# Kernel optimization log

Measured on AMD Instinct MI355X. Metric: run time of the kernel, lower is better.

## Reference

```python
import jax, jax.numpy as jnp
import numpy as np

EMBED_DIM = 768
HIDDEN_DIM = 768
ASPECT_NUM = 32
BATCH = 256


def setup_inputs() -> dict:
    key = jax.random.key(0)
    k1, k2, k3, k4, k5, k6, k7 = jax.random.split(key, 7)
    s = 0.02
    return {
        "v_X": jax.random.normal(k1, (BATCH, EMBED_DIM), dtype=jnp.float32),
        "v_H": jax.random.normal(k2, (BATCH, HIDDEN_DIM), dtype=jnp.float32),
        "aspect_ids": jax.random.randint(k3, (BATCH,), 0, ASPECT_NUM, dtype=jnp.int64),
        "W1_embs": s * jax.random.normal(k4, (ASPECT_NUM, (EMBED_DIM + HIDDEN_DIM) * HIDDEN_DIM), dtype=jnp.float32),
        "b1_embs": s * jax.random.normal(k5, (ASPECT_NUM, HIDDEN_DIM), dtype=jnp.float32),
        "W2_embs": s * jax.random.normal(k6, (ASPECT_NUM, HIDDEN_DIM * 2), dtype=jnp.float32),
        "b2_embs": s * jax.random.normal(k7, (ASPECT_NUM, 2), dtype=jnp.float32),
    }


def reference(v_X, v_H, aspect_ids, W1_embs, b1_embs, W2_embs, b2_embs):
    batch = v_X.shape[0]
    V = jnp.concatenate([v_X, v_H], axis=-1)  # (B, E+H)
    W1 = W1_embs[aspect_ids].reshape(batch, EMBED_DIM + HIDDEN_DIM, HIDDEN_DIM)
    b1 = b1_embs[aspect_ids]                  # (B, H)
    W2 = W2_embs[aspect_ids].reshape(batch, HIDDEN_DIM, 2)
    b2 = b2_embs[aspect_ids]                  # (B, 2)
    out1 = jax.nn.relu(jnp.einsum('bd,bdh->bh', V, W1) + b1)  # per-sample GEMV
    logits = jnp.einsum('bh,bht->bt', out1, W2) + b2
    return logits
```

## Files before the change

kernel.cpp:

```cpp
#include <hip/hip_runtime.h>
#include <hip/hip_bf16.h>

#define EMBED 768
#define HID 768
#define DTOT 1536
#define NASP 32
#define BATCHN 256
#define CH 16
#define MAXCHUNK 48
#define NTILE 6
#define DSPLIT 8
#define DROWS (DTOT / DSPLIT)

__global__ __launch_bounds__(256, 4) void gemv1_kernel(
    const float* __restrict__ vX, const float* __restrict__ vH,
    const float* __restrict__ W1, const int* __restrict__ aspect_ids,
    float* __restrict__ part)
{
    __shared__ int wcnt[4][NASP];
    __shared__ int basearr[NASP];
    __shared__ int countsarr[NASP];
    __shared__ int chasp[MAXCHUNK];
    __shared__ int smpall[MAXCHUNK][CH];
    __shared__ int nchunks_s;
    __shared__ __align__(16) float Vs[DROWS][CH];
    __shared__ __align__(16) float4 red[512];

    int t = threadIdx.x;
    int lane = t & 63;
    int wave = t >> 6;
    int myaid = aspect_ids[t];

    unsigned long long mymask = 0ull;
    for (int a = 0; a < NASP; ++a) {
        bool p = (myaid == a);
        unsigned long long m = __ballot(p);
        if (p) mymask = m;
        if (lane == a) wcnt[wave][a] = __popcll(m);
    }
    __syncthreads();
    if (t < NASP) {
        int ctot = wcnt[0][t] + wcnt[1][t] + wcnt[2][t] + wcnt[3][t];
        countsarr[t] = ctot;
        int nc = (ctot + CH - 1) / CH;
        int incl = nc;
        #pragma unroll
        for (int off = 1; off < NASP; off <<= 1) {
            int v = __shfl_up(incl, off, 64);
            if (t >= off) incl += v;
        }
        int base = incl - nc;
        basearr[t] = base;
        for (int j = 0; j < nc; ++j) chasp[base + j] = t;
        if (t == NASP - 1) nchunks_s = incl;
    }
    __syncthreads();
    {
        int pre = 0;
        for (int w2 = 0; w2 < wave; ++w2) pre += wcnt[w2][myaid];
        int r = pre + __popcll(mymask & ((1ull << lane) - 1ull));
        int c = basearr[myaid] + r / CH;
        smpall[c][r % CH] = t;
    }
    __syncthreads();

    int bid = blockIdx.x;
    int chunk = bid / (NTILE * DSPLIT);
    if (chunk >= nchunks_s) return;
    int rem  = bid % (NTILE * DSPLIT);
    int tile = rem / DSPLIT;
    int dsp  = rem % DSPLIT;

    int aspect = chasp[chunk];
    int cnt = countsarr[aspect] - CH * (chunk - basearr[aspect]);
    if (cnt > CH) cnt = CH;

    int dbase = dsp * DROWS;

    #pragma unroll
    for (int r = 0; r < 3; ++r) {
        int id = t + r * 256;
        int s = id & (CH - 1);
        int f = id >> 4;
        int smp = (s < cnt) ? smpall[chunk][s] : smpall[chunk][0];
        int d = dbase + f * 4;
        const float* src = (dbase < EMBED)
            ? (vX + (size_t)smp * EMBED + d)
            : (vH + (size_t)smp * HID + (d - EMBED));
        float4 v = *(const float4*)src;
        Vs[f * 4 + 0][s] = v.x;
        Vs[f * 4 + 1][s] = v.y;
        Vs[f * 4 + 2][s] = v.z;
        Vs[f * 4 + 3][s] = v.w;
    }
    __syncthreads();

    int c32 = t & 31;
    int dg  = t >> 5;
    int h   = tile * 128 + c32 * 4;

    const float* wp = W1 + (size_t)aspect * ((size_t)DTOT * HID)
                         + (size_t)(dbase + dg) * HID + h;

    float4 acc[CH];
    #pragma unroll
    for (int s = 0; s < CH; ++s) { acc[s].x = acc[s].y = acc[s].z = acc[s].w = 0.f; }

    #pragma unroll 4
    for (int k = 0; k < DROWS / 8; ++k) {
        float4 w = *(const float4*)wp;
        wp += 8 * HID;
        int d = k * 8 + dg;
        float4 va = *(const float4*)&Vs[d][0];
        float4 vb = *(const float4*)&Vs[d][4];
        float4 vc = *(const float4*)&Vs[d][8];
        float4 vd = *(const float4*)&Vs[d][12];
        acc[0].x  += va.x * w.x; acc[0].y  += va.x * w.y; acc[0].z  += va.x * w.z; acc[0].w  += va.x * w.w;
        acc[1].x  += va.y * w.x; acc[1].y  += va.y * w.y; acc[1].z  += va.y * w.z; acc[1].w  += va.y * w.w;
        acc[2].x  += va.z * w.x; acc[2].y  += va.z * w.y; acc[2].z  += va.z * w.z; acc[2].w  += va.z * w.w;
        acc[3].x  += va.w * w.x; acc[3].y  += va.w * w.y; acc[3].z  += va.w * w.z; acc[3].w  += va.w * w.w;
        acc[4].x  += vb.x * w.x; acc[4].y  += vb.x * w.y; acc[4].z  += vb.x * w.z; acc[4].w  += vb.x * w.w;
        acc[5].x  += vb.y * w.x; acc[5].y  += vb.y * w.y; acc[5].z  += vb.y * w.z; acc[5].w  += vb.y * w.w;
        acc[6].x  += vb.z * w.x; acc[6].y  += vb.z * w.y; acc[6].z  += vb.z * w.z; acc[6].w  += vb.z * w.w;
        acc[7].x  += vb.w * w.x; acc[7].y  += vb.w * w.y; acc[7].z  += vb.w * w.z; acc[7].w  += vb.w * w.w;
        acc[8].x  += vc.x * w.x; acc[8].y  += vc.x * w.y; acc[8].z  += vc.x * w.z; acc[8].w  += vc.x * w.w;
        acc[9].x  += vc.y * w.x; acc[9].y  += vc.y * w.y; acc[9].z  += vc.y * w.z; acc[9].w  += vc.y * w.w;
        acc[10].x += vc.z * w.x; acc[10].y += vc.z * w.y; acc[10].z += vc.z * w.z; acc[10].w += vc.z * w.w;
        acc[11].x += vc.w * w.x; acc[11].y += vc.w * w.y; acc[11].z += vc.w * w.z; acc[11].w += vc.w * w.w;
        acc[12].x += vd.x * w.x; acc[12].y += vd.x * w.y; acc[12].z += vd.x * w.z; acc[12].w += vd.x * w.w;
        acc[13].x += vd.y * w.x; acc[13].y += vd.y * w.y; acc[13].z += vd.y * w.z; acc[13].w += vd.y * w.w;
        acc[14].x += vd.z * w.x; acc[14].y += vd.z * w.y; acc[14].z += vd.z * w.z; acc[14].w += vd.z * w.w;
        acc[15].x += vd.w * w.x; acc[15].y += vd.w * w.y; acc[15].z += vd.w * w.z; acc[15].w += vd.w * w.w;
    }

    size_t dsp_off = (size_t)dsp * BATCHN * HID;
    #pragma unroll
    for (int sp = 0; sp < CH / 2; ++sp) {
        __syncthreads();
        red[t]       = acc[2 * sp + 0];
        red[256 + t] = acc[2 * sp + 1];
        __syncthreads();
        if (t < 64) {
            int half = t >> 5;
            int l32  = t & 31;
            int s = 2 * sp + half;
            float4 sum = red[half * 256 + l32];
            #pragma unroll
            for (int g = 1; g < 8; ++g) {
                float4 o = red[half * 256 + g * 32 + l32];
                sum.x += o.x; sum.y += o.y; sum.z += o.z; sum.w += o.w;
            }
            if (s < cnt) {
                int smp = smpall[chunk][s];
                *(float4*)&part[dsp_off + (size_t)smp * HID + tile * 128 + l32 * 4] = sum;
            }
        }
    }
}

__global__ __launch_bounds__(64) void head_kernel(
    const float* __restrict__ part, const int* __restrict__ aspect_ids,
    const float* __restrict__ b1, const float* __restrict__ W2,
    const float* __restrict__ b2, float* __restrict__ logits)
{
    int s = blockIdx.x;
    int t = threadIdx.x;
    int a = aspect_ids[s];
    const float* w2 = W2 + (size_t)a * HID * 2;
    const float* b1p = b1 + (size_t)a * HID;
    float p0 = 0.f, p1 = 0.f;
    #pragma unroll
    for (int j = 0; j < HID / 64; ++j) {
        int hh = t + j * 64;
        float o = 0.f;
        #pragma unroll
        for (int p = 0; p < DSPLIT; ++p) {
            o += part[(size_t)p * BATCHN * HID + (size_t)s * HID + hh];
        }
        o = fmaxf(o + b1p[hh], 0.f);
        p0 += o * w2[hh * 2 + 0];
        p1 += o * w2[hh * 2 + 1];
    }
    #pragma unroll
    for (int off = 32; off > 0; off >>= 1) {
        p0 += __shfl_down(p0, off, 64);
        p1 += __shfl_down(p1, off, 64);
    }
    if (t == 0) {
        logits[s * 2 + 0] = p0 + b2[a * 2 + 0];
        logits[s * 2 + 1] = p1 + b2[a * 2 + 1];
    }
}

extern "C" void kernel_launch(void* const* d_in, const int* in_sizes, int n_in,
                              void* d_out, int out_size, void* d_ws, size_t ws_size,
                              hipStream_t stream) {
    const float* vX  = (const float*)d_in[0];
    const float* vH  = (const float*)d_in[1];
    const int*   aid = (const int*)d_in[2];
    const float* W1  = (const float*)d_in[3];
    const float* b1  = (const float*)d_in[4];
    const float* W2  = (const float*)d_in[5];
    const float* b2  = (const float*)d_in[6];
    float* logits = (float*)d_out;

    float* part = (float*)d_ws;

    gemv1_kernel<<<MAXCHUNK * NTILE * DSPLIT, 256, 0, stream>>>(vX, vH, W1, aid, part);
    head_kernel<<<BATCHN, 64, 0, stream>>>(part, aid, b1, W2, b2, logits);
}
```

Before: 40.09 us.

## Fuse bias, ReLU and second layer into GEMV by removing the D-split

```diff
diff --git a/kernel.cpp b/kernel.cpp
--- a/kernel.cpp
+++ b/kernel.cpp
@@ -8,14 +8,18 @@
 #define BATCHN 256
 #define CH 16
 #define MAXCHUNK 48
-#define NTILE 6
-#define DSPLIT 8
-#define DROWS (DTOT / DSPLIT)
-
-__global__ __launch_bounds__(256, 4) void gemv1_kernel(
+#define COLS 32
+#define NT2 (HID / COLS)
+#define SROWS 192
+#define NSTAGE (DTOT / SROWS)
+#define VSP 20
+
+
+__global__ __launch_bounds__(256, 4) void gemv_fused_kernel(
     const float* __restrict__ vX, const float* __restrict__ vH,
     const float* __restrict__ W1, const int* __restrict__ aspect_ids,
-    float* __restrict__ part)
+    const float* __restrict__ b1, const float* __restrict__ W2,
+    float* __restrict__ plog)
 {
     __shared__ int wcnt[4][NASP];
     __shared__ int basearr[NASP];
@@ -23,8 +27,8 @@
     __shared__ int chasp[MAXCHUNK];
     __shared__ int smpall[MAXCHUNK][CH];
     __shared__ int nchunks_s;
-    __shared__ __align__(16) float Vs[DROWS][CH];
-    __shared__ __align__(16) float4 red[512];
+    __shared__ __align__(16) float Vs[SROWS * VSP];
+    __shared__ __align__(16) float4 redw[8][4][8];
 
     int t = threadIdx.x;
     int lane = t & 63;
@@ -57,7 +61,7 @@
     __syncthreads();
     {
         int pre = 0;
-        for (int w2 = 0; w2 < wave; ++w2) pre += wcnt[w2][myaid];
+        for (int w = 0; w < wave; ++w) pre += wcnt[w][myaid];
         int r = pre + __popcll(mymask & ((1ull << lane) - 1ull));
         int c = basearr[myaid] + r / CH;
         smpall[c][r % CH] = t;
@@ -65,131 +69,143 @@
     __syncthreads();
 
     int bid = blockIdx.x;
-    int chunk = bid / (NTILE * DSPLIT);
+    int chunk = bid / NT2;
     if (chunk >= nchunks_s) return;
-    int rem  = bid % (NTILE * DSPLIT);
-    int tile = rem / DSPLIT;
-    int dsp  = rem % DSPLIT;
+    int tile = bid % NT2;
 
     int aspect = chasp[chunk];
     int cnt = countsarr[aspect] - CH * (chunk - basearr[aspect]);
     if (cnt > CH) cnt = CH;
 
-    int dbase = dsp * DROWS;
-
-    #pragma unroll
-    for (int r = 0; r < 3; ++r) {
-        int id = t + r * 256;
-        int s = id & (CH - 1);
-        int f = id >> 4;
-        int smp = (s < cnt) ? smpall[chunk][s] : smpall[chunk][0];
-        int d = dbase + f * 4;
-        const float* src = (dbase < EMBED)
-            ? (vX + (size_t)smp * EMBED + d)
-            : (vH + (size_t)smp * HID + (d - EMBED));
-        float4 v = *(const float4*)src;
-        Vs[f * 4 + 0][s] = v.x;
-        Vs[f * 4 + 1][s] = v.y;
-        Vs[f * 4 + 2][s] = v.z;
-        Vs[f * 4 + 3][s] = v.w;
-    }
-    __syncthreads();
-
-    int c32 = t & 31;
-    int dg  = t >> 5;
-    int h   = tile * 128 + c32 * 4;
+    int c8 = t & 7;
+    int dg = t >> 3;
 
     const float* wp = W1 + (size_t)aspect * ((size_t)DTOT * HID)
-                         + (size_t)(dbase + dg) * HID + h;
+                         + (size_t)dg * HID + tile * COLS + c8 * 4;
 
     float4 acc[CH];
     #pragma unroll
     for (int s = 0; s < CH; ++s) { acc[s].x = acc[s].y = acc[s].z = acc[s].w = 0.f; }
 
-    #pragma unroll 4
-    for (int k = 0; k < DROWS / 8; ++k) {
-        float4 w = *(const float4*)wp;
-        wp += 8 * HID;
-        int d = k * 8 + dg;
-        float4 va = *(const float4*)&Vs[d][0];
-        float4 vb = *(const float4*)&Vs[d][4];
-        float4 vc = *(const float4*)&Vs[d][8];
-        float4 vd = *(const float4*)&Vs[d][12];
-        acc[0].x  += va.x * w.x; acc[0].y  += va.x * w.y; acc[0].z  += va.x * w.z; acc[0].w  += va.x * w.w;
-        acc[1].x  += va.y * w.x; acc[1].y  += va.y * w.y; acc[1].z  += va.y * w.z; acc[1].w  += va.y * w.w;
-        acc[2].x  += va.z * w.x; acc[2].y  += va.z * w.y; acc[2].z  += va.z * w.z; acc[2].w  += va.z * w.w;
-        acc[3].x  += va.w * w.x; acc[3].y  += va.w * w.y; acc[3].z  += va.w * w.z; acc[3].w  += va.w * w.w;
-        acc[4].x  += vb.x * w.x; acc[4].y  += vb.x * w.y; acc[4].z  += vb.x * w.z; acc[4].w  += vb.x * w.w;
-        acc[5].x  += vb.y * w.x; acc[5].y  += vb.y * w.y; acc[5].z  += vb.y * w.z; acc[5].w  += vb.y * w.w;
-        acc[6].x  += vb.z * w.x; acc[6].y  += vb.z * w.y; acc[6].z  += vb.z * w.z; acc[6].w  += vb.z * w.w;
-        acc[7].x  += vb.w * w.x; acc[7].y  += vb.w * w.y; acc[7].z  += vb.w * w.z; acc[7].w  += vb.w * w.w;
-        acc[8].x  += vc.x * w.x; acc[8].y  += vc.x * w.y; acc[8].z  += vc.x * w.z; acc[8].w  += vc.x * w.w;
-        acc[9].x  += vc.y * w.x; acc[9].y  += vc.y * w.y; acc[9].z  += vc.y * w.z; acc[9].w  += vc.y * w.w;
-        acc[10].x += vc.z * w.x; acc[10].y += vc.z * w.y; acc[10].z += vc.z * w.z; acc[10].w += vc.z * w.w;
-        acc[11].x += vc.w * w.x; acc[11].y += vc.w * w.y; acc[11].z += vc.w * w.z; acc[11].w += vc.w * w.w;
-        acc[12].x += vd.x * w.x; acc[12].y += vd.x * w.y; acc[12].z += vd.x * w.z; acc[12].w += vd.x * w.w;
-        acc[13].x += vd.y * w.x; acc[13].y += vd.y * w.y; acc[13].z += vd.y * w.z; acc[13].w += vd.y * w.w;
-        acc[14].x += vd.z * w.x; acc[14].y += vd.z * w.y; acc[14].z += vd.z * w.z; acc[14].w += vd.z * w.w;
-        acc[15].x += vd.w * w.x; acc[15].y += vd.w * w.y; acc[15].z += vd.w * w.z; acc[15].w += vd.w * w.w;
-    }
-
-    size_t dsp_off = (size_t)dsp * BATCHN * HID;
-    #pragma unroll
-    for (int sp = 0; sp < CH / 2; ++sp) {
-        __syncthreads();
-        red[t]       = acc[2 * sp + 0];
-        red[256 + t] = acc[2 * sp + 1];
-        __syncthreads();
-        if (t < 64) {
-            int half = t >> 5;
-            int l32  = t & 31;
-            int s = 2 * sp + half;
-            float4 sum = red[half * 256 + l32];
+    for (int st = 0; st < NSTAGE; ++st) {
+        int dbase = st * SROWS;
+        __syncthreads();
+        #pragma unroll
+        for (int r = 0; r < 3; ++r) {
+            int id = t + r * 256;
+            int s = id & (CH - 1);
+            int f = id >> 4;
+            int smp = (s < cnt) ? smpall[chunk][s] : smpall[chunk][0];
+            int d = dbase + f * 4;
+            const float* src = (dbase < EMBED)
+                ? (vX + (size_t)smp * EMBED + d)
+                : (vH + (size_t)smp * HID + (d - EMBED));
+            float4 v = *(const float4*)src;
+            Vs[(f * 4 + 0) * VSP + s] = v.x;
+            Vs[(f * 4 + 1) * VSP + s] = v.y;
+            Vs[(f * 4 + 2) * VSP + s] = v.z;
+            Vs[(f * 4 + 3) * VSP + s] = v.w;
+        }
+        __syncthreads();
+
+        #pragma unroll
+        for (int kk = 0; kk < SROWS / 32; ++kk) {
+            float4 w = *(const float4*)wp;
+            wp += 32 * HID;
+            const float* vrow = &Vs[(kk * 32 + dg) * VSP];
+            float4 va = *(const float4*)(vrow + 0);
+            float4 vb = *(const float4*)(vrow + 4);
+            float4 vc = *(const float4*)(vrow + 8);
+            float4 vd = *(const float4*)(vrow + 12);
+            acc[0].x  += va.x * w.x; acc[0].y  += va.x * w.y; acc[0].z  += va.x * w.z; acc[0].w  += va.x * w.w;
+            acc[1].x  += va.y * w.x; acc[1].y  += va.y * w.y; acc[1].z  += va.y * w.z; acc[1].w  += va.y * w.w;
+            acc[2].x  += va.z * w.x; acc[2].y  += va.z * w.y; acc[2].z  += va.z * w.z; acc[2].w  += va.z * w.w;
+            acc[3].x  += va.w * w.x; acc[3].y  += va.w * w.y; acc[3].z  += va.w * w.z; acc[3].w  += va.w * w.w;
+            acc[4].x  += vb.x * w.x; acc[4].y  += vb.x * w.y; acc[4].z  += vb.x * w.z; acc[4].w  += vb.x * w.w;
+            acc[5].x  += vb.y * w.x; acc[5].y  += vb.y * w.y; acc[5].z  += vb.y * w.z; acc[5].w  += vb.y * w.w;
+            acc[6].x  += vb.z * w.x; acc[6].y  += vb.z * w.y; acc[6].z  += vb.z * w.z; acc[6].w  += vb.z * w.w;
+            acc[7].x  += vb.w * w.x; acc[7].y  += vb.w * w.y; acc[7].z  += vb.w * w.z; acc[7].w  += vb.w * w.w;
+            acc[8].x  += vc.x * w.x; acc[8].y  += vc.x * w.y; acc[8].z  += vc.x * w.z; acc[8].w  += vc.x * w.w;
+            acc[9].x  += vc.y * w.x; acc[9].y  += vc.y * w.y; acc[9].z  += vc.y * w.z; acc[9].w  += vc.y * w.w;
+            acc[10].x += vc.z * w.x; acc[10].y += vc.z * w.y; acc[10].z += vc.z * w.z; acc[10].w += vc.z * w.w;
+            acc[11].x += vc.w * w.x; acc[11].y += vc.w * w.y; acc[11].z += vc.w * w.z; acc[11].w += vc.w * w.w;
+            acc[12].x += vd.x * w.x; acc[12].y += vd.x * w.y; acc[12].z += vd.x * w.z; acc[12].w += vd.x * w.w;
+            acc[13].x += vd.y * w.x; acc[13].y += vd.y * w.y; acc[13].z += vd.y * w.z; acc[13].w += vd.y * w.w;
+            acc[14].x += vd.z * w.x; acc[14].y += vd.z * w.y; acc[14].z += vd.z * w.z; acc[14].w += vd.z * w.w;
+            acc[15].x += vd.w * w.x; acc[15].y += vd.w * w.y; acc[15].z += vd.w * w.z; acc[15].w += vd.w * w.w;
+        }
+    }
+
+    #pragma unroll
+    for (int s = 0; s < CH; ++s) {
+        float4 v = acc[s];
+        v.x += __shfl_down(v.x, 32, 64); v.y += __shfl_down(v.y, 32, 64);
+        v.z += __shfl_down(v.z, 32, 64); v.w += __shfl_down(v.w, 32, 64);
+        v.x += __shfl_down(v.x, 16, 64); v.y += __shfl_down(v.y, 16, 64);
+        v.z += __shfl_down(v.z, 16, 64); v.w += __shfl_down(v.w, 16, 64);
+        v.x += __shfl_down(v.x,  8, 64); v.y += __shfl_down(v.y,  8, 64);
+        v.z += __shfl_down(v.z,  8, 64); v.w += __shfl_down(v.w,  8, 64);
+        acc[s] = v;
+    }
+
+    const float* b1p = b1 + (size_t)aspect * HID;
+    const float* w2p = W2 + (size_t)aspect * HID * 2;
+    #pragma unroll
+    for (int rr = 0; rr < 2; ++rr) {
+        __syncthreads();
+        if (lane < 8) {
             #pragma unroll
-            for (int g = 1; g < 8; ++g) {
-                float4 o = red[half * 256 + g * 32 + l32];
-                sum.x += o.x; sum.y += o.y; sum.z += o.z; sum.w += o.w;
+            for (int j = 0; j < 8; ++j)
+                redw[j][wave][lane] = acc[rr * 8 + j];
+        }
+        __syncthreads();
+        if (wave == 0) {
+            int j = t >> 3;
+            int c = t & 7;
+            int s = rr * 8 + j;
+            float4 a0 = redw[j][0][c], a1 = redw[j][1][c];
+            float4 a2 = redw[j][2][c], a3 = redw[j][3][c];
+            float4 sum;
+            sum.x = a0.x + a1.x + a2.x + a3.x;
+            sum.y = a0.y + a1.y + a2.y + a3.y;
+            sum.z = a0.z + a1.z + a2.z + a3.z;
+            sum.w = a0.w + a1.w + a2.w + a3.w;
+            int h = tile * COLS + c * 4;
+            float p0 = 0.f, p1 = 0.f;
+            if (s < cnt) {
+                float o;
+                o = fmaxf(sum.x + b1p[h + 0], 0.f); p0 += o * w2p[(h + 0) * 2]; p1 += o * w2p[(h + 0) * 2 + 1];
+                o = fmaxf(sum.y + b1p[h + 1], 0.f); p0 += o * w2p[(h + 1) * 2]; p1 += o * w2p[(h + 1) * 2 + 1];
+                o = fmaxf(sum.z + b1p[h + 2], 0.f); p0 += o * w2p[(h + 2) * 2]; p1 += o * w2p[(h + 2) * 2 + 1];
+                o = fmaxf(sum.w + b1p[h + 3], 0.f); p0 += o * w2p[(h + 3) * 2]; p1 += o * w2p[(h + 3) * 2 + 1];
             }
-            if (s < cnt) {
+            p0 += __shfl_down(p0, 4, 64); p1 += __shfl_down(p1, 4, 64);
+            p0 += __shfl_down(p0, 2, 64); p1 += __shfl_down(p1, 2, 64);
+            p0 += __shfl_down(p0, 1, 64); p1 += __shfl_down(p1, 1, 64);
+            if (c == 0 && s < cnt) {
                 int smp = smpall[chunk][s];
-                *(float4*)&part[dsp_off + (size_t)smp * HID + tile * 128 + l32 * 4] = sum;
+                float2 pv; pv.x = p0; pv.y = p1;
+                *(float2*)&plog[((size_t)tile * BATCHN + smp) * 2] = pv;
             }
         }
     }
 }
 
-__global__ __launch_bounds__(64) void head_kernel(
-    const float* __restrict__ part, const int* __restrict__ aspect_ids,
-    const float* __restrict__ b1, const float* __restrict__ W2,
+__global__ __launch_bounds__(BATCHN) void combine_kernel(
+    const float* __restrict__ plog, const int* __restrict__ aspect_ids,
     const float* __restrict__ b2, float* __restrict__ logits)
 {
-    int s = blockIdx.x;
-    int t = threadIdx.x;
-    int a = aspect_ids[s];
-    const float* w2 = W2 + (size_t)a * HID * 2;
-    const float* b1p = b1 + (size_t)a * HID;
-    float p0 = 0.f, p1 = 0.f;
-    #pragma unroll
-    for (int j = 0; j < HID / 64; ++j) {
-        int hh = t + j * 64;
-        float o = 0.f;
-        #pragma unroll
-        for (int p = 0; p < DSPLIT; ++p) {
-            o += part[(size_t)p * BATCHN * HID + (size_t)s * HID + hh];
-        }
-        o = fmaxf(o + b1p[hh], 0.f);
-        p0 += o * w2[hh * 2 + 0];
-        p1 += o * w2[hh * 2 + 1];
-    }
-    #pragma unroll
-    for (int off = 32; off > 0; off >>= 1) {
-        p0 += __shfl_down(p0, off, 64);
-        p1 += __shfl_down(p1, off, 64);
-    }
-    if (t == 0) {
-        logits[s * 2 + 0] = p0 + b2[a * 2 + 0];
-        logits[s * 2 + 1] = p1 + b2[a * 2 + 1];
-    }
+    int smp = threadIdx.x;
+    int a = aspect_ids[smp];
+    float p0 = b2[a * 2 + 0], p1 = b2[a * 2 + 1];
+    const float2* pl = (const float2*)plog;
+    #pragma unroll
+    for (int tl = 0; tl < NT2; ++tl) {
+        float2 v = pl[(size_t)tl * BATCHN + smp];
+        p0 += v.x; p1 += v.y;
+    }
+    float2 out; out.x = p0; out.y = p1;
+    *(float2*)&logits[smp * 2] = out;
 }
 
 extern "C" void kernel_launch(void* const* d_in, const int* in_sizes, int n_in,
@@ -204,8 +220,9 @@
     const float* b2  = (const float*)d_in[6];
     float* logits = (float*)d_out;
 
-    float* part = (float*)d_ws;
-
-    gemv1_kernel<<<MAXCHUNK * NTILE * DSPLIT, 256, 0, stream>>>(vX, vH, W1, aid, part);
-    head_kernel<<<BATCHN, 64, 0, stream>>>(part, aid, b1, W2, b2, logits);
+    float* plog = (float*)d_ws;
+
+    gemv_fused_kernel<<<MAXCHUNK * NT2, 256, 0, stream>>>(
+        vX, vH, W1, aid, b1, W2, plog);
+    combine_kernel<<<1, BATCHN, 0, stream>>>(plog, aid, b2, logits);
 }
```

Result: slower. 48.58 us (+21.2%).

## Halve D-split, stage V in shared-memory chunks, reduce via shuffles

Applied to the files above, without the earlier changes.

```diff
diff --git a/kernel.cpp b/kernel.cpp
--- a/kernel.cpp
+++ b/kernel.cpp
@@ -9,8 +9,9 @@
 #define CH 16
 #define MAXCHUNK 48
 #define NTILE 6
-#define DSPLIT 8
+#define DSPLIT 4
 #define DROWS (DTOT / DSPLIT)
+#define SROWS 192
 
 __global__ __launch_bounds__(256, 4) void gemv1_kernel(
     const float* __restrict__ vX, const float* __restrict__ vH,
@@ -23,8 +24,8 @@
     __shared__ int chasp[MAXCHUNK];
     __shared__ int smpall[MAXCHUNK][CH];
     __shared__ int nchunks_s;
-    __shared__ __align__(16) float Vs[DROWS][CH];
-    __shared__ __align__(16) float4 red[512];
+    __shared__ __align__(16) float Vs[SROWS][CH];
+    __shared__ __align__(16) float4 red[4][4][32];
 
     int t = threadIdx.x;
     int lane = t & 63;
@@ -57,7 +58,7 @@
     __syncthreads();
     {
         int pre = 0;
-        for (int w2 = 0; w2 < wave; ++w2) pre += wcnt[w2][myaid];
+        for (int w = 0; w < wave; ++w) pre += wcnt[w][myaid];
         int r = pre + __popcll(mymask & ((1ull << lane) - 1ull));
         int c = basearr[myaid] + r / CH;
         smpall[c][r % CH] = t;
@@ -75,84 +76,97 @@
     int cnt = countsarr[aspect] - CH * (chunk - basearr[aspect]);
     if (cnt > CH) cnt = CH;
 
-    int dbase = dsp * DROWS;
-
-    #pragma unroll
-    for (int r = 0; r < 3; ++r) {
-        int id = t + r * 256;
-        int s = id & (CH - 1);
-        int f = id >> 4;
-        int smp = (s < cnt) ? smpall[chunk][s] : smpall[chunk][0];
-        int d = dbase + f * 4;
-        const float* src = (dbase < EMBED)
-            ? (vX + (size_t)smp * EMBED + d)
-            : (vH + (size_t)smp * HID + (d - EMBED));
-        float4 v = *(const float4*)src;
-        Vs[f * 4 + 0][s] = v.x;
-        Vs[f * 4 + 1][s] = v.y;
-        Vs[f * 4 + 2][s] = v.z;
-        Vs[f * 4 + 3][s] = v.w;
-    }
-    __syncthreads();
-
     int c32 = t & 31;
     int dg  = t >> 5;
-    int h   = tile * 128 + c32 * 4;
 
     const float* wp = W1 + (size_t)aspect * ((size_t)DTOT * HID)
-                         + (size_t)(dbase + dg) * HID + h;
+                         + (size_t)(dsp * DROWS + dg) * HID + tile * 128 + c32 * 4;
 
     float4 acc[CH];
     #pragma unroll
     for (int s = 0; s < CH; ++s) { acc[s].x = acc[s].y = acc[s].z = acc[s].w = 0.f; }
 
-    #pragma unroll 4
-    for (int k = 0; k < DROWS / 8; ++k) {
-        float4 w = *(const float4*)wp;
-        wp += 8 * HID;
-        int d = k * 8 + dg;
-        float4 va = *(const float4*)&Vs[d][0];
-        float4 vb = *(const float4*)&Vs[d][4];
-        float4 vc = *(const float4*)&Vs[d][8];
-        float4 vd = *(const float4*)&Vs[d][12];
-        acc[0].x  += va.x * w.x; acc[0].y  += va.x * w.y; acc[0].z  += va.x * w.z; acc[0].w  += va.x * w.w;
-        acc[1].x  += va.y * w.x; acc[1].y  += va.y * w.y; acc[1].z  += va.y * w.z; acc[1].w  += va.y * w.w;
-        acc[2].x  += va.z * w.x; acc[2].y  += va.z * w.y; acc[2].z  += va.z * w.z; acc[2].w  += va.z * w.w;
-        acc[3].x  += va.w * w.x; acc[3].y  += va.w * w.y; acc[3].z  += va.w * w.z; acc[3].w  += va.w * w.w;
-        acc[4].x  += vb.x * w.x; acc[4].y  += vb.x * w.y; acc[4].z  += vb.x * w.z; acc[4].w  += vb.x * w.w;
-        acc[5].x  += vb.y * w.x; acc[5].y  += vb.y * w.y; acc[5].z  += vb.y * w.z; acc[5].w  += vb.y * w.w;
-        acc[6].x  += vb.z * w.x; acc[6].y  += vb.z * w.y; acc[6].z  += vb.z * w.z; acc[6].w  += vb.z * w.w;
-        acc[7].x  += vb.w * w.x; acc[7].y  += vb.w * w.y; acc[7].z  += vb.w * w.z; acc[7].w  += vb.w * w.w;
-        acc[8].x  += vc.x * w.x; acc[8].y  += vc.x * w.y; acc[8].z  += vc.x * w.z; acc[8].w  += vc.x * w.w;
-        acc[9].x  += vc.y * w.x; acc[9].y  += vc.y * w.y; acc[9].z  += vc.y * w.z; acc[9].w  += vc.y * w.w;
-        acc[10].x += vc.z * w.x; acc[10].y += vc.z * w.y; acc[10].z += vc.z * w.z; acc[10].w += vc.z * w.w;
-        acc[11].x += vc.w * w.x; acc[11].y += vc.w * w.y; acc[11].z += vc.w * w.z; acc[11].w += vc.w * w.w;
-        acc[12].x += vd.x * w.x; acc[12].y += vd.x * w.y; acc[12].z += vd.x * w.z; acc[12].w += vd.x * w.w;
-        acc[13].x += vd.y * w.x; acc[13].y += vd.y * w.y; acc[13].z += vd.y * w.z; acc[13].w += vd.y * w.w;
-        acc[14].x += vd.z * w.x; acc[14].y += vd.z * w.y; acc[14].z += vd.z * w.z; acc[14].w += vd.z * w.w;
-        acc[15].x += vd.w * w.x; acc[15].y += vd.w * w.y; acc[15].z += vd.w * w.z; acc[15].w += vd.w * w.w;
+    for (int st = 0; st < DROWS / SROWS; ++st) {
+        int dbase = dsp * DROWS + st * SROWS;
+        __syncthreads();
+        #pragma unroll
+        for (int r = 0; r < 3; ++r) {
+            int id = t + r * 256;
+            int s = id & (CH - 1);
+            int f = id >> 4;
+            int smp = (s < cnt) ? smpall[chunk][s] : smpall[chunk][0];
+            int d = dbase + f * 4;
+            const float* src = (dbase < EMBED)
+                ? (vX + (size_t)smp * EMBED + d)
+                : (vH + (size_t)smp * HID + (d - EMBED));
+            float4 v = *(const float4*)src;
+            Vs[f * 4 + 0][s] = v.x;
+            Vs[f * 4 + 1][s] = v.y;
+            Vs[f * 4 + 2][s] = v.z;
+            Vs[f * 4 + 3][s] = v.w;
+        }
+        __syncthreads();
+
+        #pragma unroll 4
+        for (int k = 0; k < SROWS / 8; ++k) {
+            float4 w = *(const float4*)wp;
+            wp += 8 * HID;
+            int d = k * 8 + dg;
+            float4 va = *(const float4*)&Vs[d][0];
+            float4 vb = *(const float4*)&Vs[d][4];
+            float4 vc = *(const float4*)&Vs[d][8];
+            float4 vd = *(const float4*)&Vs[d][12];
+            acc[0].x  += va.x * w.x; acc[0].y  += va.x * w.y; acc[0].z  += va.x * w.z; acc[0].w  += va.x * w.w;
+            acc[1].x  += va.y * w.x; acc[1].y  += va.y * w.y; acc[1].z  += va.y * w.z; acc[1].w  += va.y * w.w;
+            acc[2].x  += va.z * w.x; acc[2].y  += va.z * w.y; acc[2].z  += va.z * w.z; acc[2].w  += va.z * w.w;
+            acc[3].x  += va.w * w.x; acc[3].y  += va.w * w.y; acc[3].z  += va.w * w.z; acc[3].w  += va.w * w.w;
+            acc[4].x  += vb.x * w.x; acc[4].y  += vb.x * w.y; acc[4].z  += vb.x * w.z; acc[4].w  += vb.x * w.w;
+            acc[5].x  += vb.y * w.x; acc[5].y  += vb.y * w.y; acc[5].z  += vb.y * w.z; acc[5].w  += vb.y * w.w;
+            acc[6].x  += vb.z * w.x; acc[6].y  += vb.z * w.y; acc[6].z  += vb.z * w.z; acc[6].w  += vb.z * w.w;
+            acc[7].x  += vb.w * w.x; acc[7].y  += vb.w * w.y; acc[7].z  += vb.w * w.z; acc[7].w  += vb.w * w.w;
+            acc[8].x  += vc.x * w.x; acc[8].y  += vc.x * w.y; acc[8].z  += vc.x * w.z; acc[8].w  += vc.x * w.w;
+            acc[9].x  += vc.y * w.x; acc[9].y  += vc.y * w.y; acc[9].z  += vc.y * w.z; acc[9].w  += vc.y * w.w;
+            acc[10].x += vc.z * w.x; acc[10].y += vc.z * w.y; acc[10].z += vc.z * w.z; acc[10].w += vc.z * w.w;
+            acc[11].x += vc.w * w.x; acc[11].y += vc.w * w.y; acc[11].z += vc.w * w.z; acc[11].w += vc.w * w.w;
+            acc[12].x += vd.x * w.x; acc[12].y += vd.x * w.y; acc[12].z += vd.x * w.z; acc[12].w += vd.x * w.w;
+            acc[13].x += vd.y * w.x; acc[13].y += vd.y * w.y; acc[13].z += vd.y * w.z; acc[13].w += vd.y * w.w;
+            acc[14].x += vd.z * w.x; acc[14].y += vd.z * w.y; acc[14].z += vd.z * w.z; acc[14].w += vd.z * w.w;
+            acc[15].x += vd.w * w.x; acc[15].y += vd.w * w.y; acc[15].z += vd.w * w.z; acc[15].w += vd.w * w.w;
+        }
+    }
+
+    #pragma unroll
+    for (int s = 0; s < CH; ++s) {
+        float4 v = acc[s];
+        v.x += __shfl_down(v.x, 32, 64); v.y += __shfl_down(v.y, 32, 64);
+        v.z += __shfl_down(v.z, 32, 64); v.w += __shfl_down(v.w, 32, 64);
+        acc[s] = v;
     }
 
     size_t dsp_off = (size_t)dsp * BATCHN * HID;
     #pragma unroll
-    for (int sp = 0; sp < CH / 2; ++sp) {
-        __syncthreads();
-        red[t]       = acc[2 * sp + 0];
-        red[256 + t] = acc[2 * sp + 1];
-        __syncthreads();
-        if (t < 64) {
-            int half = t >> 5;
-            int l32  = t & 31;
-            int s = 2 * sp + half;
-            float4 sum = red[half * 256 + l32];
+    for (int rr = 0; rr < 4; ++rr) {
+        __syncthreads();
+        if (lane < 32) {
             #pragma unroll
-            for (int g = 1; g < 8; ++g) {
-                float4 o = red[half * 256 + g * 32 + l32];
-                sum.x += o.x; sum.y += o.y; sum.z += o.z; sum.w += o.w;
-            }
+            for (int j = 0; j < 4; ++j)
+                red[j][wave][lane] = acc[rr * 4 + j];
+        }
+        __syncthreads();
+        if (t < 128) {
+            int j = t >> 5;
+            int c = t & 31;
+            int s = rr * 4 + j;
+            float4 a0 = red[j][0][c], a1 = red[j][1][c];
+            float4 a2 = red[j][2][c], a3 = red[j][3][c];
+            float4 sum;
+            sum.x = a0.x + a1.x + a2.x + a3.x;
+            sum.y = a0.y + a1.y + a2.y + a3.y;
+            sum.z = a0.z + a1.z + a2.z + a3.z;
+            sum.w = a0.w + a1.w + a2.w + a3.w;
             if (s < cnt) {
                 int smp = smpall[chunk][s];
-                *(float4*)&part[dsp_off + (size_t)smp * HID + tile * 128 + l32 * 4] = sum;
+                *(float4*)&part[dsp_off + (size_t)smp * HID + tile * 128 + c * 4] = sum;
             }
         }
     }
```

After: 43.83 us. +9.3%, slower.
